# Optimization experiments

Measured on AMD Instinct MI355X. Metric: run time of the kernel, lower is better.

Reference implementation:

```python
import jax, jax.numpy as jnp
import numpy as np

B, N, D, F, OUT = 2048, 784, 10, 2, 10
EPS = 1e-12


def setup_inputs() -> dict:
    key = jax.random.key(0)
    k1, k2, k3, k4 = jax.random.split(key, 4)
    x = jax.random.uniform(k1, (B, N), dtype=jnp.float32)  # pixel values in [0,1]
    # xavier-uniform-like init matching the torch module's std formulas
    std0 = (2.0 / (F + F * D)) ** 0.5
    core0 = jax.random.uniform(k2, (1, F, D), jnp.float32, -std0, std0)
    stdm = (2.0 / (D * F + F * D)) ** 0.5
    cores_mid = jax.random.uniform(k3, (N - 1, D, F, D), jnp.float32, -stdm, stdm)
    classifier = jax.random.normal(k4, (OUT, D), jnp.float32) * 0.1
    return {"x": x, "core0": core0, "cores_mid": cores_mid, "classifier": classifier}


def reference(x, core0, cores_mid, classifier):
    Bsz = x.shape[0]
    xf = x.reshape(Bsz, -1)                      # [B, N]
    feats = jnp.stack([1.0 - xf, xf], axis=-1)   # [B, N, F] feature map

    # per-site contraction of cores with features (all sites at once)
    head = jnp.einsum('ldh,bd->blh', core0, feats[:, 0])            # [B, 1, D]
    tail = jnp.einsum('nldh,bnd->bnlh', cores_mid, feats[:, 1:])    # [B, N-1, D, D]

    log_norm = jnp.zeros(Bsz, dtype=x.dtype)
    # log-depth binary tree contraction; shapes shrink by ~half each level
    # (static shapes per level -> Python while is jit-compatible)
    while tail.shape[1] > 0:
        # pair 0: head (left-boundary tensor) with next tensor
        nh = head @ tail[:, 0]                                      # [B, 1, D]
        hn = jnp.maximum(jnp.sqrt(jnp.sum(nh * nh, axis=(-2, -1))), EPS)
        log_norm = log_norm + jnp.log(hn)
        head = nh / hn[:, None, None]
        # remaining tensors paired (t1,t2),(t3,t4),... ; odd leftover is carried
        rest = tail[:, 1:]
        p = rest.shape[1] // 2
        a = rest[:, 0:2 * p:2]                                      # [B, p, D, D]
        b = rest[:, 1:2 * p:2]                                      # [B, p, D, D]
        c = a @ b                                                   # [B, p, D, D]
        norms = jnp.maximum(jnp.sqrt(jnp.sum(c * c, axis=(-2, -1))), EPS)  # [B, p]
        log_norm = log_norm + jnp.sum(jnp.log(norms), axis=1)
        c = c / norms[..., None, None]
        tail = jnp.concatenate([c, rest[:, 2 * p:]], axis=1)
    mps_output = head[:, 0]                                         # [B, D]
    logits = mps_output @ classifier.T + log_norm[:, None]          # [B, OUT]
    return logits
```

## Files before the change

kernel.cpp:

```cpp
#include <hip/hip_runtime.h>


constexpr int Bsz = 2048;
constexpr int Nn  = 784;
constexpr int NS  = 783;
constexpr int LCH = 8;
constexpr int NCH = (NS + LCH - 1) / LCH;

#define PKH_FMA(d, a, b, c) \
  asm("v_pk_fma_f16 %0, %1, %2, %3" : "=v"(d) : "v"(a), "v"(b), "v"(c))
#define PKH_ACC_LO(d, m, s) \
  asm("v_pk_fma_f16 %0, %1, %2, %0 op_sel:[0,0,0] op_sel_hi:[1,0,1]" \
      : "+v"(d) : "v"(m), "v"(s))
#define PKH_ACC_HI(d, m, s) \
  asm("v_pk_fma_f16 %0, %1, %2, %0 op_sel:[0,1,0] op_sel_hi:[1,1,1]" \
      : "+v"(d) : "v"(m), "v"(s))
#define PKH_MUL_LO(d, m, s) \
  asm("v_pk_mul_f16 %0, %1, %2 op_sel:[0,0] op_sel_hi:[1,0]" \
      : "=v"(d) : "v"(m), "v"(s))
#define CVT_H2F(f, u) asm("v_cvt_f32_f16 %0, %1" : "=v"(f) : "v"(u))

__device__ __forceinline__ unsigned short f2h_bits(float f) {
    union { _Float16 h; unsigned short u; } c;
    c.h = (_Float16)f;
    return c.u;
}
__device__ __forceinline__ float hlo(unsigned u) {
    union { unsigned short s; _Float16 h; } c;
    c.s = (unsigned short)(u & 0xffff);
    return (float)c.h;
}
__device__ __forceinline__ float hhi(unsigned u) {
    union { unsigned short s; _Float16 h; } c;
    c.s = (unsigned short)(u >> 16);
    return (float)c.h;
}

__device__ __forceinline__ void site_step(const unsigned* __restrict__ ws,
                                          const unsigned x2,
                                          const unsigned (&src)[5][5],
                                          unsigned (&dst)[5][5]) {
#pragma unroll
    for (int ip = 0; ip < 5; ++ip) {
        unsigned m[10];
        const uint4* w4 = (const uint4*)(ws + ip * 20);
#pragma unroll
        for (int t = 0; t < 5; ++t) {
            const uint4 w = w4[t];
            PKH_FMA(m[2 * t],     w.y, x2, w.x);
            PKH_FMA(m[2 * t + 1], w.w, x2, w.z);
        }
#pragma unroll
        for (int r = 0; r < 5; ++r) {
            if (ip == 0) {
#pragma unroll
                for (int q = 0; q < 5; ++q) PKH_MUL_LO(dst[r][q], m[q], src[r][0]);
            } else {
#pragma unroll
                for (int q = 0; q < 5; ++q) PKH_ACC_LO(dst[r][q], m[q], src[r][ip]);
            }
#pragma unroll
            for (int q = 0; q < 5; ++q) PKH_ACC_HI(dst[r][q], m[5 + q], src[r][ip]);
        }
    }
}

__global__ __launch_bounds__(256, 4) void chunk_kernel(
    const float* __restrict__ x, const float* __restrict__ cores,
    unsigned* __restrict__ pbuf, float* __restrict__ lbuf) {
    __shared__ unsigned s_w[LCH * 100];
    __shared__ float    s_x[128 * 9];

    const int c   = blockIdx.y;
    const int n0  = 1 + c * LCH;
    const int n1  = min(n0 + LCH, Nn);
    const int ns  = n1 - n0;
    const int tid = (int)threadIdx.x;
    const int b0  = (int)blockIdx.x * 128;

    for (int e = tid; e < ns * 50; e += 256) {
        const int k = e / 50, s = e - k * 50;
        const int i = s / 5, q = s - i * 5;
        const float* g = cores + (size_t)(n0 - 1 + k) * 200 + i * 20 + 2 * q;
        const float a0 = g[0], a1 = g[1], bb0 = g[10], bb1 = g[11];
        const unsigned A = ((unsigned)f2h_bits(2.f * a1) << 16) | f2h_bits(2.f * a0);
        const unsigned D = ((unsigned)f2h_bits(2.f * (bb1 - a1)) << 16) |
                           f2h_bits(2.f * (bb0 - a0));
        s_w[k * 100 + 2 * s]     = A;
        s_w[k * 100 + 2 * s + 1] = D;
    }
    for (int e = tid; e < 128 * 8; e += 256) {
        const int bl = e >> 3, k = e & 7;
        if (k < ns) s_x[bl * 9 + k] = x[(size_t)(b0 + bl) * Nn + n0 + k];
    }
    __syncthreads();

    const int h = tid & 1;
    const int u = tid >> 1;
    const int b = b0 + u;
    const float* __restrict__ xs = s_x + u * 9;

    unsigned p[5][5], q2[5][5];
    {
        const unsigned short xb = f2h_bits(xs[0]);
        const unsigned x2 = ((unsigned)xb << 16) | xb;
#pragma unroll
        for (int r = 0; r < 5; ++r)
#pragma unroll
            for (int q = 0; q < 5; ++q) {
                const unsigned A = s_w[(5 * h + r) * 10 + 2 * q];
                const unsigned D = s_w[(5 * h + r) * 10 + 2 * q + 1];
                PKH_FMA(p[r][q], D, x2, A);
            }
    }
    int k = 1;
    while (k + 1 < ns) {
        {
            const unsigned short xb = f2h_bits(xs[k]);
            site_step(s_w + k * 100, ((unsigned)xb << 16) | xb, p, q2);
        }
        {
            const unsigned short xb = f2h_bits(xs[k + 1]);
            site_step(s_w + (k + 1) * 100, ((unsigned)xb << 16) | xb, q2, p);
        }
        k += 2;
    }
    if (k < ns) {
        const unsigned short xb = f2h_bits(xs[k]);
        site_step(s_w + k * 100, ((unsigned)xb << 16) | xb, p, q2);
#pragma unroll
        for (int r = 0; r < 5; ++r)
#pragma unroll
            for (int q = 0; q < 5; ++q) p[r][q] = q2[r][q];
    }

    float ss = 0.f;
#pragma unroll
    for (int r = 0; r < 5; ++r)
#pragma unroll
        for (int q = 0; q < 5; ++q) {
            const float lo = hlo(p[r][q]), hi = hhi(p[r][q]);
            ss = fmaf(lo, lo, ss);
            ss = fmaf(hi, hi, ss);
        }
    ss += __shfl_xor(ss, 1);
    ss = fmaxf(ss, 1e-30f);
    const float rin = rsqrtf(ss);
    if (h == 0)
        lbuf[(size_t)c * Bsz + b] = 0.5f * __logf(ss) - (float)ns * 0.69314718056f;

    unsigned* dst = pbuf + ((size_t)c * Bsz + b) * 50;
#pragma unroll
    for (int r = 0; r < 5; ++r)
#pragma unroll
        for (int q = 0; q < 5; ++q) {
            const float lo = hlo(p[r][q]) * rin;
            const float hi = hhi(p[r][q]) * rin;
            dst[(5 * h + r) * 5 + q] =
                ((unsigned)f2h_bits(hi) << 16) | f2h_bits(lo);
        }
}

__global__ __launch_bounds__(64, 1) void combine_kernel(
    const float* __restrict__ x, const float* __restrict__ core0,
    const float* __restrict__ cls, const unsigned* __restrict__ pbuf,
    const float* __restrict__ lbuf, float* __restrict__ out, int C) {
    __shared__ __align__(16) unsigned ring[8][256];

    const int tid   = (int)threadIdx.x;
    const int j     = tid & 15;
    const int jj    = (j < 10) ? j : 9;
    const int gbase = tid & 48;
    const int sl    = tid >> 4;
    const int b     = (int)blockIdx.x * 4 + sl;
    const int qoff  = jj >> 1;
    const unsigned sh = (unsigned)(jj & 1) * 16;

    float v[10];
    const float x0 = x[(size_t)b * Nn];
#pragma unroll
    for (int i = 0; i < 10; ++i) {
        const float c0 = core0[i], c1 = core0[10 + i];
        v[i] = fmaf(x0, c1 - c0, c0);
    }
    float llog = 0.f;
    for (int cc = j; cc < C; cc += 16)
        llog += lbuf[(size_t)cc * Bsz + b];
    llog += __shfl_xor(llog, 1);
    llog += __shfl_xor(llog, 2);
    llog += __shfl_xor(llog, 4);
    llog += __shfl_xor(llog, 8);

    const int flat = (tid * 4 <= 196) ? tid * 4 : 196;
    const unsigned* gsrc0 = pbuf + (size_t)blockIdx.x * 200 + flat;
    const size_t cstride = (size_t)Bsz * 50;

#define STAGE(cc)                                                          \
    __builtin_amdgcn_global_load_lds(                                      \
        (const __attribute__((address_space(1))) unsigned*)(gsrc0 +        \
            (size_t)(cc) * cstride),                                       \
        (__attribute__((address_space(3))) unsigned*)&ring[(cc) & 7][0],   \
        16, 0, 0)

#pragma unroll
    for (int d = 0; d < 7; ++d) STAGE(d);

    const int lbase = sl * 50 + qoff;

#define CONSUME(UARR, cc)                                                  \
    {                                                                      \
        float acc = 0.f;                                                   \
        _Pragma("unroll")                                                  \
        for (int i = 0; i < 10; ++i) {                                     \
            float wv;                                                      \
            CVT_H2F(wv, UARR[i]);                                          \
            acc = fmaf(v[i], wv, acc);                                     \
        }                                                                  \
        if (j >= 10) acc = 0.f;                                            \
        if (((cc) & 7) == 7 || (cc) == C - 1) {                            \
            float s = acc * acc;                                           \
            s += __shfl_xor(s, 1);                                         \
            s += __shfl_xor(s, 2);                                         \
            s += __shfl_xor(s, 4);                                         \
            s += __shfl_xor(s, 8);                                         \
            s = fmaxf(s, 1e-30f);                                          \
            llog += 0.5f * __logf(s);                                      \
            acc *= rsqrtf(s);                                              \
        }                                                                  \
        _Pragma("unroll")                                                  \
        for (int i = 0; i < 10; ++i) v[i] = __shfl(acc, gbase + i);        \
    }

#define RINGREAD(UARR, cc)                                                 \
    {                                                                      \
        const unsigned* rp = &ring[(cc) & 7][lbase];                       \
        _Pragma("unroll")                                                  \
        for (int i = 0; i < 10; ++i) UARR[i] = rp[i * 5] >> sh;            \
    }

    unsigned uA[10], uB[10];
    asm volatile("s_waitcnt vmcnt(6)" ::: "memory");
    RINGREAD(uA, 0);

    for (int c = 0; c < C; c += 2) {
        if (c + 1 < C) {
            if (c + 8 < C) {
                asm volatile("s_waitcnt vmcnt(5)" ::: "memory");
            } else {
                asm volatile("s_waitcnt vmcnt(0)" ::: "memory");
            }
            RINGREAD(uB, c + 1);
        }
        CONSUME(uA, c);
        if (c + 7 < C) STAGE(c + 7);
        if (c + 1 >= C) break;

        if (c + 2 < C) {
            if (c + 9 < C) {
                asm volatile("s_waitcnt vmcnt(5)" ::: "memory");
            } else {
                asm volatile("s_waitcnt vmcnt(0)" ::: "memory");
            }
            RINGREAD(uA, c + 2);
        }
        CONSUME(uB, c + 1);
        if (c + 8 < C) STAGE(c + 8);
    }
#undef RINGREAD
#undef CONSUME
#undef STAGE

    if (j < 10) {
        float acc = llog;
#pragma unroll
        for (int i = 0; i < 10; ++i) acc = fmaf(v[i], cls[j * 10 + i], acc);
        out[(size_t)b * 10 + j] = acc;
    }
}

extern "C" void kernel_launch(void* const* d_in, const int* in_sizes, int n_in,
                              void* d_out, int out_size, void* d_ws, size_t ws_size,
                              hipStream_t stream) {
    const float* x     = (const float*)d_in[0];
    const float* core0 = (const float*)d_in[1];
    const float* cores = (const float*)d_in[2];
    const float* cls   = (const float*)d_in[3];
    float* out = (float*)d_out;

    const int C = NCH;
    unsigned* pbuf = (unsigned*)d_ws;
    float*    lbuf = (float*)(pbuf + (size_t)C * Bsz * 50);

    hipLaunchKernelGGL(chunk_kernel, dim3(Bsz / 128, C), dim3(256),
                       0, stream, x, cores, pbuf, lbuf);
    hipLaunchKernelGGL(combine_kernel, dim3(Bsz / 4), dim3(64),
                       0, stream, x, core0, cls, pbuf, lbuf, out, C);
}
```

Baseline: 80.32 us.

## Double chunk length and restructure site step to update product rows in place

Raises the number of sites per chunk from 8 to 16, which halves the number of chunks and so the partial-product traffic and later combine work. The per-site step now computes all 50 site-matrix words up front, then updates the 5x5 packed-half product one row at a time through a 5-word accumulator. This removes the second full 25-register ping-pong buffer. In exchange each thread runs a longer serial chain, there are fewer blocks for parallelism, and fp16 accumulates over more sites before renormalization.

```diff
diff --git a/kernel.cpp b/kernel.cpp
--- a/kernel.cpp
+++ b/kernel.cpp
@@ -4,7 +4,7 @@
 constexpr int Bsz = 2048;
 constexpr int Nn  = 784;
 constexpr int NS  = 783;
-constexpr int LCH = 8;
+constexpr int LCH = 16;
 constexpr int NCH = (NS + LCH - 1) / LCH;
 
 #define PKH_FMA(d, a, b, c) \
@@ -36,40 +36,11 @@
     return (float)c.h;
 }
 
-__device__ __forceinline__ void site_step(const unsigned* __restrict__ ws,
-                                          const unsigned x2,
-                                          const unsigned (&src)[5][5],
-                                          unsigned (&dst)[5][5]) {
-#pragma unroll
-    for (int ip = 0; ip < 5; ++ip) {
-        unsigned m[10];
-        const uint4* w4 = (const uint4*)(ws + ip * 20);
-#pragma unroll
-        for (int t = 0; t < 5; ++t) {
-            const uint4 w = w4[t];
-            PKH_FMA(m[2 * t],     w.y, x2, w.x);
-            PKH_FMA(m[2 * t + 1], w.w, x2, w.z);
-        }
-#pragma unroll
-        for (int r = 0; r < 5; ++r) {
-            if (ip == 0) {
-#pragma unroll
-                for (int q = 0; q < 5; ++q) PKH_MUL_LO(dst[r][q], m[q], src[r][0]);
-            } else {
-#pragma unroll
-                for (int q = 0; q < 5; ++q) PKH_ACC_LO(dst[r][q], m[q], src[r][ip]);
-            }
-#pragma unroll
-            for (int q = 0; q < 5; ++q) PKH_ACC_HI(dst[r][q], m[5 + q], src[r][ip]);
-        }
-    }
-}
-
 __global__ __launch_bounds__(256, 4) void chunk_kernel(
     const float* __restrict__ x, const float* __restrict__ cores,
     unsigned* __restrict__ pbuf, float* __restrict__ lbuf) {
     __shared__ unsigned s_w[LCH * 100];
-    __shared__ float    s_x[128 * 9];
+    __shared__ float    s_x[128 * 17];
 
     const int c   = blockIdx.y;
     const int n0  = 1 + c * LCH;
@@ -89,18 +60,18 @@
         s_w[k * 100 + 2 * s]     = A;
         s_w[k * 100 + 2 * s + 1] = D;
     }
-    for (int e = tid; e < 128 * 8; e += 256) {
-        const int bl = e >> 3, k = e & 7;
-        if (k < ns) s_x[bl * 9 + k] = x[(size_t)(b0 + bl) * Nn + n0 + k];
+    for (int e = tid; e < 128 * 16; e += 256) {
+        const int bl = e >> 4, k = e & 15;
+        if (k < ns) s_x[bl * 17 + k] = x[(size_t)(b0 + bl) * Nn + n0 + k];
     }
     __syncthreads();
 
     const int h = tid & 1;
     const int u = tid >> 1;
     const int b = b0 + u;
-    const float* __restrict__ xs = s_x + u * 9;
-
-    unsigned p[5][5], q2[5][5];
+    const float* __restrict__ xs = s_x + u * 17;
+
+    unsigned p[5][5];
     {
         const unsigned short xb = f2h_bits(xs[0]);
         const unsigned x2 = ((unsigned)xb << 16) | xb;
@@ -113,25 +84,45 @@
                 PKH_FMA(p[r][q], D, x2, A);
             }
     }
-    int k = 1;
-    while (k + 1 < ns) {
-        {
-            const unsigned short xb = f2h_bits(xs[k]);
-            site_step(s_w + k * 100, ((unsigned)xb << 16) | xb, p, q2);
-        }
-        {
-            const unsigned short xb = f2h_bits(xs[k + 1]);
-            site_step(s_w + (k + 1) * 100, ((unsigned)xb << 16) | xb, q2, p);
-        }
-        k += 2;
-    }
-    if (k < ns) {
+
+    for (int k = 1; k < ns; ++k) {
         const unsigned short xb = f2h_bits(xs[k]);
-        site_step(s_w + k * 100, ((unsigned)xb << 16) | xb, p, q2);
-#pragma unroll
-        for (int r = 0; r < 5; ++r)
-#pragma unroll
-            for (int q = 0; q < 5; ++q) p[r][q] = q2[r][q];
+        const unsigned x2 = ((unsigned)xb << 16) | xb;
+        const unsigned* ws = s_w + k * 100;
+
+        unsigned Mf[50];
+#pragma unroll
+        for (int ip = 0; ip < 5; ++ip) {
+            const uint4* w4 = (const uint4*)(ws + ip * 20);
+#pragma unroll
+            for (int t = 0; t < 5; ++t) {
+                const uint4 w = w4[t];
+                PKH_FMA(Mf[ip * 10 + 2 * t],     w.y, x2, w.x);
+                PKH_FMA(Mf[ip * 10 + 2 * t + 1], w.w, x2, w.z);
+            }
+        }
+
+#pragma unroll
+        for (int r = 0; r < 5; ++r) {
+            unsigned acc[5];
+#pragma unroll
+            for (int q = 0; q < 5; ++q)
+                PKH_MUL_LO(acc[q], Mf[q], p[r][0]);
+#pragma unroll
+            for (int q = 0; q < 5; ++q)
+                PKH_ACC_HI(acc[q], Mf[5 + q], p[r][0]);
+#pragma unroll
+            for (int ip = 1; ip < 5; ++ip) {
+#pragma unroll
+                for (int q = 0; q < 5; ++q)
+                    PKH_ACC_LO(acc[q], Mf[ip * 10 + q], p[r][ip]);
+#pragma unroll
+                for (int q = 0; q < 5; ++q)
+                    PKH_ACC_HI(acc[q], Mf[ip * 10 + 5 + q], p[r][ip]);
+            }
+#pragma unroll
+            for (int q = 0; q < 5; ++q) p[r][q] = acc[q];
+        }
     }
 
     float ss = 0.f;
```

Result: faster. 72.81 us (-9.3%).
